# Performance work log

Measured on AMD Instinct MI355X. Metric: run time of the kernel, lower is better.

## Reference

```python
import jax, jax.numpy as jnp
import numpy as np

L = 32      # num_layer
N_ORD = 64  # order_of_a_LTImodel
U = 64      # u_size
Y = 64      # y_size
T = 8192    # sequence length
SCALE = 0.05  # keep block-bidiagonal A spectrally stable over 8192 steps


def setup_inputs() -> dict:
    key = jax.random.key(0)
    k_u, k_a, k_b0, k_bl, k_c = jax.random.split(key, 5)
    inp = {
        "input": jax.random.normal(k_u, (T, U), dtype=jnp.float32),
        # per-layer A_i weights (diagonal blocks)
        "A_stack": jax.random.normal(k_a, (L, N_ORD, N_ORD), dtype=jnp.float32) * SCALE,
        # layer-0 B (maps u -> state)
        "B0": jax.random.normal(k_b0, (N_ORD, U), dtype=jnp.float32) * SCALE,
        # layer i>=1 B weights (sub-diagonal coupling blocks)
        "B_lower": jax.random.normal(k_bl, (L - 1, N_ORD, N_ORD), dtype=jnp.float32) * SCALE,
        # per-layer C_i weights, concatenated along columns in forward
        "C_stack": jax.random.normal(k_c, (L, Y, N_ORD), dtype=jnp.float32),
        # D is frozen zeros (feedthrough=False)
        "D_w": jnp.zeros((Y, U), dtype=jnp.float32),
    }
    return inp


def _assemble(A_stack, B0, B_lower, C_stack):
    l, n, _ = A_stack.shape
    S = l * n
    A = jnp.zeros((S, S), A_stack.dtype)
    for i in range(l):  # fixed small structural loop
        A = A.at[i * n:(i + 1) * n, i * n:(i + 1) * n].set(A_stack[i])
    for i in range(1, l):
        A = A.at[i * n:(i + 1) * n, (i - 1) * n:i * n].set(B_lower[i - 1])
    B = jnp.concatenate([B0, jnp.zeros((S - n, B0.shape[1]), B0.dtype)], axis=0)
    # torch.cat([C_i], dim=1): [Y, L*n]
    C = jnp.transpose(C_stack, (1, 0, 2)).reshape(C_stack.shape[1], S)
    return A, B, C


def reference(input, A_stack, B0, B_lower, C_stack, D_w):
    A, B, C = _assemble(A_stack, B0, B_lower, C_stack)
    S = A.shape[0]
    x0 = jnp.zeros((S,), input.dtype)

    def step(x, u):
        y = C @ x + D_w @ u      # output BEFORE state update (y_t uses x_t)
        x_next = A @ x + B @ u
        return x_next, y

    _, ys = jax.lax.scan(step, x0, input)
    return ys  # [T, Y]
```

## Files before the change

### kernel.cpp

```cpp
#include <hip/hip_runtime.h>


#define LYR 32
#define NO  64
#define TSEQ 8192
#define JT  16
#define KD  (JT*NO)
#define PROWS (TSEQ+JT)
#define PBUF ((size_t)PROWS*NO)

typedef _Float16 h16;
typedef _Float16 h16x8 __attribute__((ext_vector_type(8)));
typedef float    f32x4 __attribute__((ext_vector_type(4)));

__global__ __launch_bounds__(256) void prep_build(
    const float* __restrict__ u, const float* __restrict__ B0,
    const float* __restrict__ Bl, const float* __restrict__ Cst,
    const float* __restrict__ Ast,
    h16* __restrict__ pall, h16* __restrict__ ccast, h16* __restrict__ kt)
{
    __shared__ float sm[3*64*68];
    const int tid = threadIdx.x;

    if (blockIdx.x < 32) {
        const int layer = blockIdx.x;
        float* la = sm;
        float* kc = sm + 64*68;
        float* kn = sm + 2*64*68;
        const float* k0 = (layer == 0) ? B0 : (Bl + (size_t)(layer-1)*4096);
        const float* Aw = Ast + (size_t)layer*4096;
        for (int e = tid; e < 4096; e += 256) {
            int r = e >> 6, c = e & 63;
            kc[r*68 + c] = k0[e];
            la[r*68 + c] = Aw[e];
        }
        __syncthreads();
        {
            size_t kb = (size_t)layer*65536 + 15*64;
            for (int e2 = tid; e2 < 1024; e2 += 256) {
                int n = e2 >> 4, c4 = (e2 & 15) << 2;
                h16 o4[4];
                #pragma unroll
                for (int t = 0; t < 4; t++) o4[t] = (h16)kc[n*68 + c4 + t];
                *(int2*)&kt[kb + (size_t)n*1024 + c4] = *(int2*)&o4[0];
            }
        }
        const int r0 = (tid >> 4) << 2;
        const int c0 = (tid & 15) << 2;
        for (int j = 1; j <= 15; j++) {
            float acc[4][4] = {};
            for (int k = 0; k < 64; k++) {
                float a0 = la[(r0+0)*68 + k];
                float a1 = la[(r0+1)*68 + k];
                float a2 = la[(r0+2)*68 + k];
                float a3 = la[(r0+3)*68 + k];
                f32x4 bv = *(const f32x4*)&kc[k*68 + c0];
                #pragma unroll
                for (int jj = 0; jj < 4; jj++) {
                    acc[0][jj] += a0*bv[jj]; acc[1][jj] += a1*bv[jj];
                    acc[2][jj] += a2*bv[jj]; acc[3][jj] += a3*bv[jj];
                }
            }
            size_t kb = (size_t)layer*65536 + (size_t)(15 - j)*64;
            #pragma unroll
            for (int i2 = 0; i2 < 4; i2++) {
                f32x4 o; o[0]=acc[i2][0]; o[1]=acc[i2][1]; o[2]=acc[i2][2]; o[3]=acc[i2][3];
                *(f32x4*)&kn[(r0+i2)*68 + c0] = o;
                h16 o4[4];
                #pragma unroll
                for (int t = 0; t < 4; t++) o4[t] = (h16)acc[i2][t];
                *(int2*)&kt[kb + (size_t)(r0+i2)*1024 + c0] = *(int2*)&o4[0];
            }
            __syncthreads();
            float* tmp = kc; kc = kn; kn = tmp;
        }
        return;
    }

    const int n_pad0 = JT*NO;
    const int n_u    = TSEQ*NO;
    const int n_c    = LYR*NO*NO;
    const int n_zp   = 32*JT*NO;
    const int total8 = (n_pad0 + n_u + n_c + n_zp) >> 3;
    int idx8 = (blockIdx.x - 32)*256 + tid;
    const int4 zero4 = make_int4(0,0,0,0);
    for (; idx8 < total8; idx8 += 512*256) {
        int e = idx8 << 3;
        if (e < n_pad0) { *(int4*)&pall[e] = zero4; continue; }
        e -= n_pad0;
        if (e < n_u) {
            f32x4 f0 = *(const f32x4*)&u[e];
            f32x4 f1 = *(const f32x4*)&u[e+4];
            h16 ov[8];
            #pragma unroll
            for (int j = 0; j < 4; j++) { ov[j] = (h16)f0[j]; ov[4+j] = (h16)f1[j]; }
            *(int4*)&pall[n_pad0 + e] = *(int4*)&ov[0];
            continue;
        }
        e -= n_u;
        if (e < n_c) {
            f32x4 f0 = *(const f32x4*)&Cst[e];
            f32x4 f1 = *(const f32x4*)&Cst[e+4];
            h16 ov[8];
            #pragma unroll
            for (int j = 0; j < 4; j++) { ov[j] = (h16)f0[j]; ov[4+j] = (h16)f1[j]; }
            *(int4*)&ccast[e] = *(int4*)&ov[0];
            continue;
        }
        e -= n_c;
        int b = e >> 10;
        int off = e & 1023;
        *(int4*)&pall[(size_t)(b+1)*PBUF + off] = zero4;
    }
}

template<int S>
__device__ __forceinline__ void phase_body(
    const h16* inb, h16* outb, const h16* __restrict__ kb,
    h16* __restrict__ gout, const int w0, float* red, const int tid)
{
    const int wv = tid >> 6, lane = tid & 63, r = lane & 15, q = lane >> 4;
    const h16* abase = inb + (r + wv*4)*72 + q*8;
    const h16* bbase = kb + (size_t)r*KD + wv*256 + q*8;
#define LDA(s, ls) (*(const h16x8*)(abase + ((s)*16 + ((ls)>>1))*72 + ((ls)&1)*32))
#define LDB(c, ls) (*(const h16x8*)(bbase + (c)*(16*KD) + (ls)*32))
    f32x4 acc[S][4] = {};
    h16x8 a[2][S], b[4][4];
    #pragma unroll
    for (int ls = 0; ls < 2; ls++)
        #pragma unroll
        for (int s = 0; s < S; s++) a[ls][s] = LDA(s, ls);
    #pragma unroll
    for (int ls = 0; ls < 4; ls++)
        #pragma unroll
        for (int c = 0; c < 4; c++) b[ls][c] = LDB(c, ls);
    #pragma unroll
    for (int ls = 0; ls < 8; ls++) {
        h16x8 ca[S], cb[4];
        #pragma unroll
        for (int s = 0; s < S; s++) ca[s] = a[ls&1][s];
        #pragma unroll
        for (int c = 0; c < 4; c++) cb[c] = b[ls&3][c];
        if (ls < 6) {
            #pragma unroll
            for (int s = 0; s < S; s++) a[ls&1][s] = LDA(s, ls+2);
        }
        if (ls < 4) {
            #pragma unroll
            for (int c = 0; c < 4; c++) b[ls&3][c] = LDB(c, ls+4);
        }
        #pragma unroll
        for (int s = 0; s < S; s++)
            #pragma unroll
            for (int c = 0; c < 4; c++)
                acc[s][c] = __builtin_amdgcn_mfma_f32_16x16x32_f16(ca[s], cb[c], acc[s][c], 0,0,0);
    }
#undef LDA
#undef LDB
    const int cb2 = (tid & 7) << 3;
    #pragma unroll
    for (int ch = 0; ch < (S+2)/3; ch++) {
        const int sbase = ch*3;
        const int nt = (S - sbase) < 3 ? (S - sbase) : 3;
        __syncthreads();
        if (wv >= 2) {
            float* myred = red + (size_t)(wv-2)*(48*68);
            #pragma unroll
            for (int s2 = 0; s2 < 3; s2++) if (s2 < nt)
                #pragma unroll
                for (int c = 0; c < 4; c++)
                    #pragma unroll
                    for (int g = 0; g < 4; g++)
                        myred[(s2*16 + q*4 + g)*68 + c*16 + r] = acc[sbase+s2][c][g];
        }
        __syncthreads();
        if (wv < 2) {
            float* myred = red + (size_t)wv*(48*68);
            #pragma unroll
            for (int s2 = 0; s2 < 3; s2++) if (s2 < nt)
                #pragma unroll
                for (int c = 0; c < 4; c++)
                    #pragma unroll
                    for (int g = 0; g < 4; g++)
                        myred[(s2*16 + q*4 + g)*68 + c*16 + r] += acc[sbase+s2][c][g];
        }
        __syncthreads();
        for (int w = tid >> 3; w < nt*16; w += 32) {
            f32x4 u0 = *(const f32x4*)&red[w*68 + cb2];
            f32x4 u1 = *(const f32x4*)&red[w*68 + cb2 + 4];
            f32x4 v0 = *(const f32x4*)&red[48*68 + w*68 + cb2];
            f32x4 v1 = *(const f32x4*)&red[48*68 + w*68 + cb2 + 4];
            u0 += v0; u1 += v1;
            h16 ov[8];
            #pragma unroll
            for (int j = 0; j < 4; j++) { ov[j] = (h16)u0[j]; ov[4+j] = (h16)u1[j]; }
            const int W = sbase*16 + w;
            if (outb) *(int4*)&outb[W*72 + cb2] = *(int4*)&ov[0];
            const unsigned wrel = (unsigned)(W - w0);
            if (wrel < 32u) *(int4*)&gout[(size_t)wrel*64 + cb2] = *(int4*)&ov[0];
        }
    }
    __syncthreads();
}

__global__ __launch_bounds__(256) void stage2(
    h16* pall, const h16* __restrict__ kt, int i0)
{
    __shared__ __align__(16) h16   bufA[64*72];
    __shared__ __align__(16) h16   bufB[48*72];
    __shared__ __align__(16) float red[2*48*68];
    const int tid = threadIdx.x;
    const size_t t0 = (size_t)blockIdx.x * 32;

    const h16* pin = pall + (size_t)i0*PBUF;
    for (int e = tid; e < 64*8; e += 256) {
        int rr = e >> 3, cc = e & 7;
        long g = (long)t0 - 16 + rr;
        int4 v = make_int4(0,0,0,0);
        if (g >= 0) v = *(const int4*)&pin[(size_t)g*64 + cc*8];
        *(int4*)&bufA[rr*72 + cc*8] = v;
    }
    __syncthreads();

    h16* g1 = pall + (size_t)(i0+1)*PBUF + (JT + t0)*64;
    h16* g2 = pall + (size_t)(i0+2)*PBUF + (JT + t0)*64;
    const h16* k1 = kt + (size_t)(i0+0)*NO*KD;
    const h16* k2 = kt + (size_t)(i0+1)*NO*KD;

    phase_body<3>(bufA, bufB, k1, g1, 16, red, tid);
    phase_body<2>(bufB, (h16*)0, k2, g2, 0, red, tid);
}

__global__ __launch_bounds__(256, 2) void y_final(
    const h16* __restrict__ pall, const h16* __restrict__ ccast,
    float* __restrict__ out)
{
    __shared__ __align__(16) float red[2*32*68];
    int tid = threadIdx.x;
    size_t t0 = (size_t)blockIdx.x * 32;
    int wv = tid >> 6, lane = tid & 63, r = lane & 15, q = lane >> 4;
    const h16* abase = pall + (size_t)(wv*8 + 1)*PBUF + (JT + t0 + r)*64 + q*8;
    const h16* bbase = ccast + (size_t)(wv*8)*4096 + (size_t)r*64 + q*8;
#define LDA2(s, ls) (*(const h16x8*)(abase + (size_t)((ls)>>1)*PBUF + (s)*(16*64) + ((ls)&1)*32))
#define LDB2(c, ls) (*(const h16x8*)(bbase + ((ls)>>1)*4096 + (c)*(16*64) + ((ls)&1)*32))
    f32x4 acc[2][4] = {};
    h16x8 a[4][2], b[4][4];
    #pragma unroll
    for (int ls = 0; ls < 4; ls++) {
        #pragma unroll
        for (int s = 0; s < 2; s++) a[ls][s] = LDA2(s, ls);
        #pragma unroll
        for (int c = 0; c < 4; c++) b[ls][c] = LDB2(c, ls);
    }
    #pragma unroll
    for (int ls = 0; ls < 16; ls++) {
        h16x8 ca[2], cb[4];
        #pragma unroll
        for (int s = 0; s < 2; s++) ca[s] = a[ls&3][s];
        #pragma unroll
        for (int c = 0; c < 4; c++) cb[c] = b[ls&3][c];
        if (ls < 12) {
            #pragma unroll
            for (int s = 0; s < 2; s++) a[ls&3][s] = LDA2(s, ls+4);
            #pragma unroll
            for (int c = 0; c < 4; c++) b[ls&3][c] = LDB2(c, ls+4);
        }
        #pragma unroll
        for (int s = 0; s < 2; s++)
            #pragma unroll
            for (int c = 0; c < 4; c++)
                acc[s][c] = __builtin_amdgcn_mfma_f32_16x16x32_f16(ca[s], cb[c], acc[s][c], 0,0,0);
    }
#undef LDA2
#undef LDB2
    if (wv >= 2) {
        float* myred = red + (size_t)(wv-2)*(32*68);
        #pragma unroll
        for (int s = 0; s < 2; s++)
            #pragma unroll
            for (int c = 0; c < 4; c++)
                #pragma unroll
                for (int g = 0; g < 4; g++)
                    myred[(s*16 + q*4 + g)*68 + c*16 + r] = acc[s][c][g];
    }
    __syncthreads();
    if (wv < 2) {
        float* myred = red + (size_t)wv*(32*68);
        #pragma unroll
        for (int s = 0; s < 2; s++)
            #pragma unroll
            for (int c = 0; c < 4; c++)
                #pragma unroll
                for (int g = 0; g < 4; g++)
                    myred[(s*16 + q*4 + g)*68 + c*16 + r] += acc[s][c][g];
    }
    __syncthreads();
    int orow = tid >> 3, cb2 = (tid & 7) << 3;
    f32x4 u0 = *(const f32x4*)&red[orow*68 + cb2];
    f32x4 u1 = *(const f32x4*)&red[orow*68 + cb2 + 4];
    f32x4 v0 = *(const f32x4*)&red[32*68 + orow*68 + cb2];
    f32x4 v1 = *(const f32x4*)&red[32*68 + orow*68 + cb2 + 4];
    u0 += v0; u1 += v1;
    size_t obase = (t0 + orow)*64 + cb2;
    *(f32x4*)&out[obase]     = u0;
    *(f32x4*)&out[obase + 4] = u1;
}

extern "C" void kernel_launch(void* const* d_in, const int* in_sizes, int n_in,
                              void* d_out, int out_size, void* d_ws, size_t ws_size,
                              hipStream_t stream)
{
    const float* u   = (const float*)d_in[0];
    const float* Ast = (const float*)d_in[1];
    const float* B0  = (const float*)d_in[2];
    const float* Bl  = (const float*)d_in[3];
    const float* Cst = (const float*)d_in[4];
    float* out = (float*)d_out;
    (void)in_sizes; (void)n_in; (void)out_size; (void)ws_size;

    char* ws = (char*)d_ws;
    const size_t PBUF_BYTES = PBUF*sizeof(h16);
    h16*   pall  = (h16*)ws;
    h16*   ccast = (h16*)(ws + 33*PBUF_BYTES);
    h16*   kt    = (h16*)(ws + 33*PBUF_BYTES + 262144);

    prep_build<<<544, 256, 0, stream>>>(u, B0, Bl, Cst, Ast, pall, ccast, kt);
    for (int i = 0; i < LYR; i += 2) {
        stage2<<<TSEQ/32, 256, 0, stream>>>(pall, kt, i);
    }
    y_final<<<TSEQ/32, 256, 0, stream>>>(pall, ccast, out);
}
```

Measured before the change: 317.9 us.

## Replace fused two-layer stage kernel with single-layer kernel per launch

```diff
diff --git a/kernel.cpp b/kernel.cpp
--- a/kernel.cpp
+++ b/kernel.cpp
@@ -114,121 +114,76 @@
     }
 }
 
-template<int S>
-__device__ __forceinline__ void phase_body(
-    const h16* inb, h16* outb, const h16* __restrict__ kb,
-    h16* __restrict__ gout, const int w0, float* red, const int tid)
-{
+__global__ __launch_bounds__(256, 2) void stage1(
+    h16* pall, const h16* __restrict__ kt, int i0)
+{
+    __shared__ __align__(16) h16   win[32*72];
+    __shared__ __align__(16) float red[2*16*68];
+    const int tid = threadIdx.x;
+    const size_t t0 = (size_t)blockIdx.x * 16;
+
+    const h16* pin = pall + (size_t)i0*PBUF;
+    for (int e = tid; e < 32*8; e += 256) {
+        int rr = e >> 3, cc = e & 7;
+        *(int4*)&win[rr*72 + cc*8] = *(const int4*)&pin[(t0 + rr)*64 + cc*8];
+    }
+    __syncthreads();
+
     const int wv = tid >> 6, lane = tid & 63, r = lane & 15, q = lane >> 4;
-    const h16* abase = inb + (r + wv*4)*72 + q*8;
-    const h16* bbase = kb + (size_t)r*KD + wv*256 + q*8;
-#define LDA(s, ls) (*(const h16x8*)(abase + ((s)*16 + ((ls)>>1))*72 + ((ls)&1)*32))
-#define LDB(c, ls) (*(const h16x8*)(bbase + (c)*(16*KD) + (ls)*32))
-    f32x4 acc[S][4] = {};
-    h16x8 a[2][S], b[4][4];
-    #pragma unroll
-    for (int ls = 0; ls < 2; ls++)
-        #pragma unroll
-        for (int s = 0; s < S; s++) a[ls][s] = LDA(s, ls);
+    const h16* abase = &win[(r + wv*4)*72 + q*8];
+    const h16* bbase = kt + (size_t)i0*NO*KD + (size_t)r*KD + wv*256 + q*8;
+#define LDA1(ls) (*(const h16x8*)(abase + ((ls)>>1)*72 + ((ls)&1)*32))
+#define LDB1(c, ls) (*(const h16x8*)(bbase + (c)*(16*KD) + (ls)*32))
+    f32x4 acc[4] = {};
+    h16x8 a[2], b[4][4];
+    a[0] = LDA1(0); a[1] = LDA1(1);
     #pragma unroll
     for (int ls = 0; ls < 4; ls++)
         #pragma unroll
-        for (int c = 0; c < 4; c++) b[ls][c] = LDB(c, ls);
+        for (int c = 0; c < 4; c++) b[ls][c] = LDB1(c, ls);
     #pragma unroll
     for (int ls = 0; ls < 8; ls++) {
-        h16x8 ca[S], cb[4];
-        #pragma unroll
-        for (int s = 0; s < S; s++) ca[s] = a[ls&1][s];
+        h16x8 ca = a[ls&1], cb[4];
         #pragma unroll
         for (int c = 0; c < 4; c++) cb[c] = b[ls&3][c];
-        if (ls < 6) {
-            #pragma unroll
-            for (int s = 0; s < S; s++) a[ls&1][s] = LDA(s, ls+2);
-        }
+        if (ls < 6) a[ls&1] = LDA1(ls+2);
         if (ls < 4) {
             #pragma unroll
-            for (int c = 0; c < 4; c++) b[ls&3][c] = LDB(c, ls+4);
-        }
-        #pragma unroll
-        for (int s = 0; s < S; s++)
-            #pragma unroll
-            for (int c = 0; c < 4; c++)
-                acc[s][c] = __builtin_amdgcn_mfma_f32_16x16x32_f16(ca[s], cb[c], acc[s][c], 0,0,0);
-    }
-#undef LDA
-#undef LDB
-    const int cb2 = (tid & 7) << 3;
-    #pragma unroll
-    for (int ch = 0; ch < (S+2)/3; ch++) {
-        const int sbase = ch*3;
-        const int nt = (S - sbase) < 3 ? (S - sbase) : 3;
-        __syncthreads();
-        if (wv >= 2) {
-            float* myred = red + (size_t)(wv-2)*(48*68);
-            #pragma unroll
-            for (int s2 = 0; s2 < 3; s2++) if (s2 < nt)
-                #pragma unroll
-                for (int c = 0; c < 4; c++)
-                    #pragma unroll
-                    for (int g = 0; g < 4; g++)
-                        myred[(s2*16 + q*4 + g)*68 + c*16 + r] = acc[sbase+s2][c][g];
-        }
-        __syncthreads();
-        if (wv < 2) {
-            float* myred = red + (size_t)wv*(48*68);
-            #pragma unroll
-            for (int s2 = 0; s2 < 3; s2++) if (s2 < nt)
-                #pragma unroll
-                for (int c = 0; c < 4; c++)
-                    #pragma unroll
-                    for (int g = 0; g < 4; g++)
-                        myred[(s2*16 + q*4 + g)*68 + c*16 + r] += acc[sbase+s2][c][g];
-        }
-        __syncthreads();
-        for (int w = tid >> 3; w < nt*16; w += 32) {
-            f32x4 u0 = *(const f32x4*)&red[w*68 + cb2];
-            f32x4 u1 = *(const f32x4*)&red[w*68 + cb2 + 4];
-            f32x4 v0 = *(const f32x4*)&red[48*68 + w*68 + cb2];
-            f32x4 v1 = *(const f32x4*)&red[48*68 + w*68 + cb2 + 4];
-            u0 += v0; u1 += v1;
-            h16 ov[8];
-            #pragma unroll
-            for (int j = 0; j < 4; j++) { ov[j] = (h16)u0[j]; ov[4+j] = (h16)u1[j]; }
-            const int W = sbase*16 + w;
-            if (outb) *(int4*)&outb[W*72 + cb2] = *(int4*)&ov[0];
-            const unsigned wrel = (unsigned)(W - w0);
-            if (wrel < 32u) *(int4*)&gout[(size_t)wrel*64 + cb2] = *(int4*)&ov[0];
-        }
-    }
-    __syncthreads();
-}
-
-__global__ __launch_bounds__(256) void stage2(
-    h16* pall, const h16* __restrict__ kt, int i0)
-{
-    __shared__ __align__(16) h16   bufA[64*72];
-    __shared__ __align__(16) h16   bufB[48*72];
-    __shared__ __align__(16) float red[2*48*68];
-    const int tid = threadIdx.x;
-    const size_t t0 = (size_t)blockIdx.x * 32;
-
-    const h16* pin = pall + (size_t)i0*PBUF;
-    for (int e = tid; e < 64*8; e += 256) {
-        int rr = e >> 3, cc = e & 7;
-        long g = (long)t0 - 16 + rr;
-        int4 v = make_int4(0,0,0,0);
-        if (g >= 0) v = *(const int4*)&pin[(size_t)g*64 + cc*8];
-        *(int4*)&bufA[rr*72 + cc*8] = v;
-    }
-    __syncthreads();
-
-    h16* g1 = pall + (size_t)(i0+1)*PBUF + (JT + t0)*64;
-    h16* g2 = pall + (size_t)(i0+2)*PBUF + (JT + t0)*64;
-    const h16* k1 = kt + (size_t)(i0+0)*NO*KD;
-    const h16* k2 = kt + (size_t)(i0+1)*NO*KD;
-
-    phase_body<3>(bufA, bufB, k1, g1, 16, red, tid);
-    phase_body<2>(bufB, (h16*)0, k2, g2, 0, red, tid);
+            for (int c = 0; c < 4; c++) b[ls&3][c] = LDB1(c, ls+4);
+        }
+        #pragma unroll
+        for (int c = 0; c < 4; c++)
+            acc[c] = __builtin_amdgcn_mfma_f32_16x16x32_f16(ca, cb[c], acc[c], 0,0,0);
+    }
+#undef LDA1
+#undef LDB1
+    if (wv >= 2) {
+        float* myred = red + (size_t)(wv-2)*(16*68);
+        #pragma unroll
+        for (int c = 0; c < 4; c++)
+            #pragma unroll
+            for (int g = 0; g < 4; g++)
+                myred[(q*4 + g)*68 + c*16 + r] = acc[c][g];
+    }
+    __syncthreads();
+    if (wv < 2) {
+        float* myred = red + (size_t)wv*(16*68);
+        #pragma unroll
+        for (int c = 0; c < 4; c++)
+            #pragma unroll
+            for (int g = 0; g < 4; g++)
+                myred[(q*4 + g)*68 + c*16 + r] += acc[c][g];
+    }
+    __syncthreads();
+    int orow = tid >> 4, c4 = (tid & 15) << 2;
+    f32x4 u0 = *(const f32x4*)&red[orow*68 + c4];
+    f32x4 v0 = *(const f32x4*)&red[16*68 + orow*68 + c4];
+    u0 += v0;
+    h16 o4[4];
+    #pragma unroll
+    for (int j = 0; j < 4; j++) o4[j] = (h16)u0[j];
+    h16* gout = pall + (size_t)(i0+1)*PBUF + (JT + t0)*64;
+    *(int2*)&gout[(size_t)orow*64 + c4] = *(int2*)&o4[0];
 }
 
 __global__ __launch_bounds__(256, 2) void y_final(
@@ -325,8 +280,8 @@
     h16*   kt    = (h16*)(ws + 33*PBUF_BYTES + 262144);
 
     prep_build<<<544, 256, 0, stream>>>(u, B0, Bl, Cst, Ast, pall, ccast, kt);
-    for (int i = 0; i < LYR; i += 2) {
-        stage2<<<TSEQ/32, 256, 0, stream>>>(pall, kt, i);
+    for (int i = 0; i < LYR; i++) {
+        stage1<<<TSEQ/16, 256, 0, stream>>>(pall, kt, i);
     }
     y_final<<<TSEQ/32, 256, 0, stream>>>(pall, ccast, out);
 }
```

Result: slower. 425.8 us (+33.9%).
